# Optimization experiments

Hardware: AMD Instinct MI355X
Metric: run time of the kernel (lower is better)

## Reference

```python
import jax, jax.numpy as jnp
import numpy as np

TOP_K = 2  # k experts per token


def setup_inputs() -> dict:
    key = jax.random.key(0)
    ks = jax.random.split(key, 6)
    B, L, D, E, F = 2, 2048, 1024, 8, 4096
    x = jax.random.normal(ks[0], (B, L, D), dtype=jnp.float32)
    Wg = jax.random.normal(ks[1], (D, E), dtype=jnp.float32) * (D ** -0.5)
    W1 = jax.random.normal(ks[2], (E, D, F), dtype=jnp.float32) * (D ** -0.5)
    b1 = jnp.zeros((E, F), dtype=jnp.float32)
    W2 = jax.random.normal(ks[3], (E, F, D), dtype=jnp.float32) * (F ** -0.5)
    b2 = jnp.zeros((E, D), dtype=jnp.float32)
    return {"x": x, "Wg": Wg, "W1": W1, "b1": b1, "W2": W2, "b2": b2}


def reference(x, Wg, W1, b1, W2, b2):
    b, l, d = x.shape
    E = Wg.shape[1]
    xt = x.reshape(b * l, d)                      # (N, D)
    N = xt.shape[0]
    # Router: sigmoid gate, top-k (gate weights are NOT renormalized in the source)
    S = jax.nn.sigmoid(xt @ Wg)                   # (N, E)
    G, I = jax.lax.top_k(S, TOP_K)                # (N, k) each
    # Dense equivalent of per-expert gather-MLP-scatter: run every expert
    # on every token, then combine with the sparse top-k routing weights.
    h = jax.nn.gelu(jnp.einsum('nd,edf->enf', xt, W1) + b1[:, None, :])  # (E, N, F)
    y = jnp.einsum('enf,efd->end', h, W2) + b2[:, None, :]               # (E, N, D)
    # combine[n, e] = sum of gate values for slots routed to expert e
    combine = jnp.zeros((N, E), dtype=x.dtype).at[jnp.arange(N)[:, None], I].add(G)
    out = jnp.einsum('ne,end->nd', combine, y)    # (N, D)
    return out.reshape(b, l, d)
```

## Files before the change

### kernel.cpp

```cpp
#include <hip/hip_runtime.h>
#include <math.h>

typedef __bf16 bf16_t;
typedef __attribute__((ext_vector_type(8))) __bf16 bf16x8;
typedef __attribute__((ext_vector_type(4))) __bf16 bf16x4;
typedef __attribute__((ext_vector_type(4))) float f32x4;

#define NTOK 4096
#define DDIM 1024
#define FDIM 4096
#define NEXP 8
#define CAP  4096
#define HROWS (2*NTOK + 128)
#define NPAIR (2*NTOK)
#define MAXB 72

#define PREP_BLOCKS 2048
#define PREP_UNITS 13312

#define GLOAD_LDS16(g, l) \
  __builtin_amdgcn_global_load_lds((__attribute__((address_space(1))) void*)(g), \
                                   (__attribute__((address_space(3))) void*)(l), 16, 0, 0)

__device__ __forceinline__ float fast_gelu(float v) {
  float u = 0.7978845608028654f * (v + 0.044715f * v * v * v);
  float uc = fminf(fmaxf(u, -10.f), 10.f);
  float t = __builtin_amdgcn_exp2f(2.885390081777927f * uc);
  float th = (t - 1.f) * __builtin_amdgcn_rcpf(t + 1.f);
  return 0.5f * v * (1.0f + th);
}

__device__ __forceinline__ void reg_transpose(const float* __restrict__ ip,
                                              bf16_t* __restrict__ op,
                                              int R, int C, int r0, int c0,
                                              int t) {
  const int w = t >> 6;
  const int lane = t & 63;
  const int g = lane >> 4;
  const int m = lane & 15;
  const int rr = r0 + w * 32 + 8 * g;
  const int cc = c0 + 4 * m;
  f32x4 v[8];
#pragma unroll
  for (int ri = 0; ri < 8; ri++)
    v[ri] = *(const f32x4*)(ip + (size_t)(rr + ri) * C + cc);
#pragma unroll
  for (int ci = 0; ci < 4; ci++) {
    bf16x8 o;
#pragma unroll
    for (int ri = 0; ri < 8; ri++) o[ri] = (bf16_t)v[ri][ci];
    *(bf16x8*)(op + (size_t)(cc + ci) * R + rr) = o;
  }
}

__global__ __launch_bounds__(256) void prep_kernel(
    const float* __restrict__ W1, const float* __restrict__ W2,
    const float* __restrict__ x, const float* __restrict__ Wg,
    bf16_t* __restrict__ wt1, bf16_t* __restrict__ wt2,
    bf16_t* __restrict__ xbf, int* __restrict__ tokL, int* __restrict__ cnts,
    int* __restrict__ pairE, int* __restrict__ pairS, float* __restrict__ pairG) {
  const int t = threadIdx.x;
  for (int u = blockIdx.x; u < PREP_UNITS; u += PREP_BLOCKS) {
    if (u < 4096) {
      int e = u >> 9, ti = u & 511;
      int r0 = (ti & 7) * 128, c0 = (ti >> 3) * 64;
      reg_transpose(W1 + (size_t)e * DDIM * FDIM, wt1 + (size_t)e * DDIM * FDIM,
                    DDIM, FDIM, r0, c0, t);
    } else if (u < 8192) {
      int b0 = u - 4096;
      int e = b0 >> 9, ti = b0 & 511;
      int r0 = (ti & 31) * 128, c0 = (ti >> 5) * 64;
      reg_transpose(W2 + (size_t)e * FDIM * DDIM, wt2 + (size_t)e * FDIM * DDIM,
                    FDIM, DDIM, r0, c0, t);
    } else if (u < 12288) {
      int i = (u - 8192) * 256 + t;
      float4 v = ((const float4*)x)[i];
      bf16x4 o;
      o.x = (bf16_t)v.x; o.y = (bf16_t)v.y; o.z = (bf16_t)v.z; o.w = (bf16_t)v.w;
      ((bf16x4*)xbf)[i] = o;
    } else {
      int b0 = u - 12288;
      int wid = t >> 6, lane = t & 63;
      int n = b0 * 4 + wid;
      const float* xr = x + (size_t)n * DDIM;
      double acc[NEXP];
#pragma unroll
      for (int e = 0; e < NEXP; e++) acc[e] = 0.0;
      for (int i = 0; i < DDIM / 64; i++) {
        int d = i * 64 + lane;
        float xv = xr[d];
        const float* wr = Wg + (size_t)d * NEXP;
#pragma unroll
        for (int e = 0; e < NEXP; e++) acc[e] += (double)xv * (double)wr[e];
      }
#pragma unroll
      for (int e = 0; e < NEXP; e++) {
        double v = acc[e];
#pragma unroll
        for (int off = 32; off; off >>= 1) v += __shfl_xor(v, off);
        acc[e] = v;
      }
      if (lane == 0) {
        int i1 = -1, i2 = -1;
        double s1 = -1e300, s2 = -1e300;
#pragma unroll
        for (int e = 0; e < NEXP; e++) {
          double v = acc[e];
          if (v > s1) { s2 = s1; i2 = i1; s1 = v; i1 = e; }
          else if (v > s2) { s2 = v; i2 = e; }
        }
        float g1 = 1.0f / (1.0f + expf((float)(-s1)));
        float g2 = 1.0f / (1.0f + expf((float)(-s2)));
        int p1 = atomicAdd(&cnts[i1], 1);
        tokL[i1 * CAP + p1] = n;
        int p2 = atomicAdd(&cnts[i2], 1);
        tokL[i2 * CAP + p2] = n;
        pairE[2 * n] = i1; pairS[2 * n] = p1; pairG[2 * n] = g1;
        pairE[2 * n + 1] = i2; pairS[2 * n + 1] = p2; pairG[2 * n + 1] = g2;
      }
    }
  }
}

__global__ void offs_kernel(const int* __restrict__ cnts, int* __restrict__ offs,
                            int* __restrict__ blkE, int* __restrict__ blkS) {
  if (threadIdx.x == 0) {
    int s = 0, nb = 0;
    for (int e = 0; e < NEXP; e++) {
      offs[e] = s;
      for (int st = 0; st < cnts[e]; st += 128) { blkE[nb] = e; blkS[nb] = st; nb++; }
      s += cnts[e];
    }
    offs[NEXP] = s;
    for (; nb < MAXB; nb++) { blkE[nb] = NEXP; blkS[nb] = 0; }
  }
}

__global__ __launch_bounds__(256) void gemm1_kernel(
    const bf16_t* __restrict__ xbf, const bf16_t* __restrict__ wt1,
    const float* __restrict__ b1, const int* __restrict__ tokL,
    const int* __restrict__ cnts, const int* __restrict__ offs,
    const int* __restrict__ blkE, const int* __restrict__ blkS,
    bf16_t* __restrict__ H) {
  const int e = blkE[blockIdx.y];
  if (e >= NEXP) return;
  const int m0 = blkS[blockIdx.y];
  const int cnt = cnts[e];
  const int n0 = blockIdx.x * 128;
  const int t = threadIdx.x;

  __shared__ alignas(16) bf16_t As[128 * 32];
  __shared__ alignas(16) bf16_t Bs[128 * 32];

  const int sr = t >> 2;
  const int sc = (t & 3) * 8;
  const int r0 = m0 + sr, r1 = m0 + sr + 64;
  const int tok0 = (r0 < cnt) ? tokL[e * CAP + r0] : 0;
  const int tok1 = (r1 < cnt) ? tokL[e * CAP + r1] : 0;
  const bf16_t* gA0 = xbf + (size_t)tok0 * DDIM + sc;
  const bf16_t* gA1 = xbf + (size_t)tok1 * DDIM + sc;
  const bf16_t* wte = wt1 + (size_t)e * FDIM * DDIM;
  const bf16_t* gB0 = wte + (size_t)(n0 + sr) * DDIM + sc;
  const bf16_t* gB1 = wte + (size_t)(n0 + sr + 64) * DDIM + sc;
  bf16_t* lA0 = As + t * 8; bf16_t* lA1 = As + 2048 + t * 8;
  bf16_t* lB0 = Bs + t * 8; bf16_t* lB1 = Bs + 2048 + t * 8;

  const int lane = t & 63, w = t >> 6;
  const int wm = (w >> 1) * 64, wn = (w & 1) * 64;
  const int lid = lane & 15, quad = lane >> 4;

  f32x4 acc[4][4] = {};
  for (int kk = 0; kk < DDIM; kk += 32) {
    GLOAD_LDS16(gA0 + kk, lA0);
    GLOAD_LDS16(gA1 + kk, lA1);
    GLOAD_LDS16(gB0 + kk, lB0);
    GLOAD_LDS16(gB1 + kk, lB1);
    __syncthreads();
    bf16x8 af[4], bfm[4];
#pragma unroll
    for (int i = 0; i < 4; i++)
      af[i] = *(const bf16x8*)(As + (wm + i * 16 + lid) * 32 + quad * 8);
#pragma unroll
    for (int j = 0; j < 4; j++)
      bfm[j] = *(const bf16x8*)(Bs + (wn + j * 16 + lid) * 32 + quad * 8);
#pragma unroll
    for (int i = 0; i < 4; i++)
#pragma unroll
      for (int j = 0; j < 4; j++)
        acc[i][j] = __builtin_amdgcn_mfma_f32_16x16x32_bf16(af[i], bfm[j], acc[i][j], 0, 0, 0);
    __syncthreads();
  }

  const float* b1e = b1 + (size_t)e * FDIM;
  const int offe = offs[e];
#pragma unroll
  for (int i = 0; i < 4; i++) {
#pragma unroll
    for (int reg = 0; reg < 4; reg++) {
      int pos = m0 + wm + i * 16 + quad * 4 + reg;
      if (pos >= cnt) continue;
      size_t hrow = (size_t)(offe + pos);
#pragma unroll
      for (int j = 0; j < 4; j++) {
        int col = n0 + wn + j * 16 + lid;
        float v = acc[i][j][reg] + b1e[col];
        H[hrow * FDIM + col] = (bf16_t)fast_gelu(v);
      }
    }
  }
}

__global__ __launch_bounds__(256) void gemm2_kernel(
    const bf16_t* __restrict__ H, const bf16_t* __restrict__ wt2,
    const int* __restrict__ cnts, const int* __restrict__ offs,
    const int* __restrict__ blkE, const int* __restrict__ blkS,
    float* __restrict__ Y0, float* __restrict__ Y1) {
  const int bi = blockIdx.y >> 1;
  const int split = blockIdx.y & 1;
  const int e = blkE[bi];
  if (e >= NEXP) return;
  const int m0 = blkS[bi];
  const int cnt = cnts[e];
  const int n0 = blockIdx.x * 128;
  const int t = threadIdx.x;
  const int offe = offs[e];
  const int k0 = split * (FDIM / 2);

  __shared__ alignas(16) bf16_t As[128 * 32];
  __shared__ alignas(16) bf16_t Bs[128 * 32];

  const int sr = t >> 2;
  const int sc = (t & 3) * 8;
  const bf16_t* gA0 = H + (size_t)(offe + m0 + sr) * FDIM + sc + k0;
  const bf16_t* gA1 = H + (size_t)(offe + m0 + sr + 64) * FDIM + sc + k0;
  const bf16_t* wte = wt2 + (size_t)e * DDIM * FDIM;
  const bf16_t* gB0 = wte + (size_t)(n0 + sr) * FDIM + sc + k0;
  const bf16_t* gB1 = wte + (size_t)(n0 + sr + 64) * FDIM + sc + k0;
  bf16_t* lA0 = As + t * 8; bf16_t* lA1 = As + 2048 + t * 8;
  bf16_t* lB0 = Bs + t * 8; bf16_t* lB1 = Bs + 2048 + t * 8;

  const int lane = t & 63, w = t >> 6;
  const int wm = (w >> 1) * 64, wn = (w & 1) * 64;
  const int lid = lane & 15, quad = lane >> 4;

  f32x4 acc[4][4] = {};
  for (int kk = 0; kk < FDIM / 2; kk += 32) {
    GLOAD_LDS16(gA0 + kk, lA0);
    GLOAD_LDS16(gA1 + kk, lA1);
    GLOAD_LDS16(gB0 + kk, lB0);
    GLOAD_LDS16(gB1 + kk, lB1);
    __syncthreads();
    bf16x8 af[4], bfm[4];
#pragma unroll
    for (int i = 0; i < 4; i++)
      af[i] = *(const bf16x8*)(As + (wm + i * 16 + lid) * 32 + quad * 8);
#pragma unroll
    for (int j = 0; j < 4; j++)
      bfm[j] = *(const bf16x8*)(Bs + (wn + j * 16 + lid) * 32 + quad * 8);
#pragma unroll
    for (int i = 0; i < 4; i++)
#pragma unroll
      for (int j = 0; j < 4; j++)
        acc[i][j] = __builtin_amdgcn_mfma_f32_16x16x32_bf16(af[i], bfm[j], acc[i][j], 0, 0, 0);
    __syncthreads();
  }

  float* Ye = split ? Y1 : Y0;
#pragma unroll
  for (int i = 0; i < 4; i++) {
#pragma unroll
    for (int reg = 0; reg < 4; reg++) {
      int pos = m0 + wm + i * 16 + quad * 4 + reg;
      if (pos >= cnt) continue;
      float* yrow = Ye + (size_t)(offe + pos) * DDIM;
#pragma unroll
      for (int j = 0; j < 4; j++) {
        int col = n0 + wn + j * 16 + lid;
        yrow[col] = acc[i][j][reg];
      }
    }
  }
}

__global__ __launch_bounds__(256) void combine_kernel(
    const float* __restrict__ Y0, const float* __restrict__ Y1,
    const float* __restrict__ b2, const int* __restrict__ pairE,
    const int* __restrict__ pairS, const float* __restrict__ pairG,
    const int* __restrict__ offs, float4* __restrict__ out4) {
  const int n = blockIdx.x;
  const int e1 = pairE[2 * n], e2 = pairE[2 * n + 1];
  const int r1 = offs[e1] + pairS[2 * n];
  const int r2 = offs[e2] + pairS[2 * n + 1];
  const float g1 = pairG[2 * n], g2 = pairG[2 * n + 1];
  const int t = threadIdx.x;
  const float4* ya0 = (const float4*)(Y0 + (size_t)r1 * DDIM);
  const float4* ya1 = (const float4*)(Y1 + (size_t)r1 * DDIM);
  const float4* yb0 = (const float4*)(Y0 + (size_t)r2 * DDIM);
  const float4* yb1 = (const float4*)(Y1 + (size_t)r2 * DDIM);
  const float4* ba = (const float4*)(b2 + (size_t)e1 * DDIM);
  const float4* bb = (const float4*)(b2 + (size_t)e2 * DDIM);
  float4 a0 = ya0[t], a1 = ya1[t], c0 = yb0[t], c1 = yb1[t];
  float4 pa = ba[t], pb = bb[t];
  float4 o;
  o.x = g1 * (a0.x + a1.x + pa.x) + g2 * (c0.x + c1.x + pb.x);
  o.y = g1 * (a0.y + a1.y + pa.y) + g2 * (c0.y + c1.y + pb.y);
  o.z = g1 * (a0.z + a1.z + pa.z) + g2 * (c0.z + c1.z + pb.z);
  o.w = g1 * (a0.w + a1.w + pa.w) + g2 * (c0.w + c1.w + pb.w);
  out4[(size_t)n * (DDIM / 4) + t] = o;
}

extern "C" void kernel_launch(void* const* d_in, const int* in_sizes, int n_in,
                              void* d_out, int out_size, void* d_ws, size_t ws_size,
                              hipStream_t stream) {
  const float* x  = (const float*)d_in[0];
  const float* Wg = (const float*)d_in[1];
  const float* W1 = (const float*)d_in[2];
  const float* b1 = (const float*)d_in[3];
  const float* W2 = (const float*)d_in[4];
  const float* b2 = (const float*)d_in[5];
  float* out = (float*)d_out;

  char* ws = (char*)d_ws;
  size_t off = 0;
  auto alloc = [&](size_t bytes) -> void* {
    void* p = (void*)(ws + off);
    off += (bytes + 255) & ~(size_t)255;
    return p;
  };
  bf16_t* xbf   = (bf16_t*)alloc((size_t)NTOK * DDIM * 2);
  bf16_t* wt1   = (bf16_t*)alloc((size_t)NEXP * FDIM * DDIM * 2);
  bf16_t* wt2   = (bf16_t*)alloc((size_t)NEXP * DDIM * FDIM * 2);
  bf16_t* H     = (bf16_t*)alloc((size_t)HROWS * FDIM * 2);
  int*    tokL  = (int*)alloc((size_t)NEXP * CAP * 4);
  int*    pairE = (int*)alloc((size_t)NPAIR * 4);
  int*    pairS = (int*)alloc((size_t)NPAIR * 4);
  float*  pairG = (float*)alloc((size_t)NPAIR * 4);
  int*    cnts  = (int*)alloc(64);
  int*    offs  = (int*)alloc(64);
  int*    blkE  = (int*)alloc(MAXB * 4);
  int*    blkS  = (int*)alloc(MAXB * 4);
  if (off > ws_size) return;

  float* Y0 = (float*)wt1;
  float* Y1 = Y0 + (size_t)8192 * DDIM;

  hipMemsetAsync(cnts, 0, 64, stream);
  prep_kernel<<<PREP_BLOCKS, 256, 0, stream>>>(W1, W2, x, Wg, wt1, wt2, xbf, tokL,
                                               cnts, pairE, pairS, pairG);
  offs_kernel<<<1, 64, 0, stream>>>(cnts, offs, blkE, blkS);
  gemm1_kernel<<<dim3(FDIM / 128, MAXB), 256, 0, stream>>>(
      xbf, wt1, b1, tokL, cnts, offs, blkE, blkS, H);
  gemm2_kernel<<<dim3(DDIM / 128, MAXB * 2), 256, 0, stream>>>(
      H, wt2, cnts, offs, blkE, blkS, Y0, Y1);
  combine_kernel<<<NTOK, 256, 0, stream>>>(Y0, Y1, b2, pairE, pairS, pairG, offs,
                                           (float4*)out);
}
```

Baseline: 670.5 us.

## Swizzle GEMM block order for L2 locality and drop gemm2 split-K

Remaps block indices in both GEMM kernels so that consecutive blocks dispatched to the same XCD share weight or activation tiles in L2. Removes the two-way split-K in the second GEMM, so each block covers the full F dimension and writes a single Y buffer. The combine kernel then reads one partial instead of two per routed slot. This cuts Y write and read traffic, but halves the gemm2 grid and doubles its per-block serial K loop, which may hurt occupancy and tail balance.

Result: slower. 685.8 us (+2.3%).

```diff
diff --git a/kernel.cpp b/kernel.cpp
--- a/kernel.cpp
+++ b/kernel.cpp
@@ -142,11 +142,15 @@
     const int* __restrict__ cnts, const int* __restrict__ offs,
     const int* __restrict__ blkE, const int* __restrict__ blkS,
     bf16_t* __restrict__ H) {
-  const int e = blkE[blockIdx.y];
+  const int bid = blockIdx.x + 32 * blockIdx.y;
+  const int swz = (bid & 7) * 288 + (bid >> 3);
+  const int by = swz % 72;
+  const int bx = swz / 72;
+  const int e = blkE[by];
   if (e >= NEXP) return;
-  const int m0 = blkS[blockIdx.y];
+  const int m0 = blkS[by];
   const int cnt = cnts[e];
-  const int n0 = blockIdx.x * 128;
+  const int n0 = bx * 128;
   const int t = threadIdx.x;
 
   __shared__ alignas(16) bf16_t As[128 * 32];
@@ -214,28 +218,29 @@
     const bf16_t* __restrict__ H, const bf16_t* __restrict__ wt2,
     const int* __restrict__ cnts, const int* __restrict__ offs,
     const int* __restrict__ blkE, const int* __restrict__ blkS,
-    float* __restrict__ Y0, float* __restrict__ Y1) {
-  const int bi = blockIdx.y >> 1;
-  const int split = blockIdx.y & 1;
-  const int e = blkE[bi];
+    float* __restrict__ Y) {
+  const int bid = blockIdx.x + 8 * blockIdx.y;
+  const int swz = (bid & 7) * 72 + (bid >> 3);
+  const int bx = swz & 7;
+  const int by = swz >> 3;
+  const int e = blkE[by];
   if (e >= NEXP) return;
-  const int m0 = blkS[bi];
+  const int m0 = blkS[by];
   const int cnt = cnts[e];
-  const int n0 = blockIdx.x * 128;
+  const int n0 = bx * 128;
   const int t = threadIdx.x;
   const int offe = offs[e];
-  const int k0 = split * (FDIM / 2);
 
   __shared__ alignas(16) bf16_t As[128 * 32];
   __shared__ alignas(16) bf16_t Bs[128 * 32];
 
   const int sr = t >> 2;
   const int sc = (t & 3) * 8;
-  const bf16_t* gA0 = H + (size_t)(offe + m0 + sr) * FDIM + sc + k0;
-  const bf16_t* gA1 = H + (size_t)(offe + m0 + sr + 64) * FDIM + sc + k0;
+  const bf16_t* gA0 = H + (size_t)(offe + m0 + sr) * FDIM + sc;
+  const bf16_t* gA1 = H + (size_t)(offe + m0 + sr + 64) * FDIM + sc;
   const bf16_t* wte = wt2 + (size_t)e * DDIM * FDIM;
-  const bf16_t* gB0 = wte + (size_t)(n0 + sr) * FDIM + sc + k0;
-  const bf16_t* gB1 = wte + (size_t)(n0 + sr + 64) * FDIM + sc + k0;
+  const bf16_t* gB0 = wte + (size_t)(n0 + sr) * FDIM + sc;
+  const bf16_t* gB1 = wte + (size_t)(n0 + sr + 64) * FDIM + sc;
   bf16_t* lA0 = As + t * 8; bf16_t* lA1 = As + 2048 + t * 8;
   bf16_t* lB0 = Bs + t * 8; bf16_t* lB1 = Bs + 2048 + t * 8;
 
@@ -244,7 +249,7 @@
   const int lid = lane & 15, quad = lane >> 4;
 
   f32x4 acc[4][4] = {};
-  for (int kk = 0; kk < FDIM / 2; kk += 32) {
+  for (int kk = 0; kk < FDIM; kk += 32) {
     GLOAD_LDS16(gA0 + kk, lA0);
     GLOAD_LDS16(gA1 + kk, lA1);
     GLOAD_LDS16(gB0 + kk, lB0);
@@ -265,14 +270,13 @@
     __syncthreads();
   }
 
-  float* Ye = split ? Y1 : Y0;
 #pragma unroll
   for (int i = 0; i < 4; i++) {
 #pragma unroll
     for (int reg = 0; reg < 4; reg++) {
       int pos = m0 + wm + i * 16 + quad * 4 + reg;
       if (pos >= cnt) continue;
-      float* yrow = Ye + (size_t)(offe + pos) * DDIM;
+      float* yrow = Y + (size_t)(offe + pos) * DDIM;
 #pragma unroll
       for (int j = 0; j < 4; j++) {
         int col = n0 + wn + j * 16 + lid;
@@ -283,29 +287,27 @@
 }
 
 __global__ __launch_bounds__(256) void combine_kernel(
-    const float* __restrict__ Y0, const float* __restrict__ Y1,
-    const float* __restrict__ b2, const int* __restrict__ pairE,
-    const int* __restrict__ pairS, const float* __restrict__ pairG,
-    const int* __restrict__ offs, float4* __restrict__ out4) {
+    const float* __restrict__ Y, const float* __restrict__ b2,
+    const int* __restrict__ pairE, const int* __restrict__ pairS,
+    const float* __restrict__ pairG, const int* __restrict__ offs,
+    float4* __restrict__ out4) {
   const int n = blockIdx.x;
   const int e1 = pairE[2 * n], e2 = pairE[2 * n + 1];
   const int r1 = offs[e1] + pairS[2 * n];
   const int r2 = offs[e2] + pairS[2 * n + 1];
   const float g1 = pairG[2 * n], g2 = pairG[2 * n + 1];
   const int t = threadIdx.x;
-  const float4* ya0 = (const float4*)(Y0 + (size_t)r1 * DDIM);
-  const float4* ya1 = (const float4*)(Y1 + (size_t)r1 * DDIM);
-  const float4* yb0 = (const float4*)(Y0 + (size_t)r2 * DDIM);
-  const float4* yb1 = (const float4*)(Y1 + (size_t)r2 * DDIM);
+  const float4* ya = (const float4*)(Y + (size_t)r1 * DDIM);
+  const float4* yb = (const float4*)(Y + (size_t)r2 * DDIM);
   const float4* ba = (const float4*)(b2 + (size_t)e1 * DDIM);
   const float4* bb = (const float4*)(b2 + (size_t)e2 * DDIM);
-  float4 a0 = ya0[t], a1 = ya1[t], c0 = yb0[t], c1 = yb1[t];
+  float4 a0 = ya[t], c0 = yb[t];
   float4 pa = ba[t], pb = bb[t];
   float4 o;
-  o.x = g1 * (a0.x + a1.x + pa.x) + g2 * (c0.x + c1.x + pb.x);
-  o.y = g1 * (a0.y + a1.y + pa.y) + g2 * (c0.y + c1.y + pb.y);
-  o.z = g1 * (a0.z + a1.z + pa.z) + g2 * (c0.z + c1.z + pb.z);
-  o.w = g1 * (a0.w + a1.w + pa.w) + g2 * (c0.w + c1.w + pb.w);
+  o.x = g1 * (a0.x + pa.x) + g2 * (c0.x + pb.x);
+  o.y = g1 * (a0.y + pa.y) + g2 * (c0.y + pb.y);
+  o.z = g1 * (a0.z + pa.z) + g2 * (c0.z + pb.z);
+  o.w = g1 * (a0.w + pa.w) + g2 * (c0.w + pb.w);
   out4[(size_t)n * (DDIM / 4) + t] = o;
 }
 
@@ -341,8 +343,7 @@
   int*    blkS  = (int*)alloc(MAXB * 4);
   if (off > ws_size) return;
 
-  float* Y0 = (float*)wt1;
-  float* Y1 = Y0 + (size_t)8192 * DDIM;
+  float* Y = (float*)wt1;
 
   hipMemsetAsync(cnts, 0, 64, stream);
   prep_kernel<<<PREP_BLOCKS, 256, 0, stream>>>(W1, W2, x, Wg, wt1, wt2, xbf, tokL,
@@ -350,8 +351,8 @@
   offs_kernel<<<1, 64, 0, stream>>>(cnts, offs, blkE, blkS);
   gemm1_kernel<<<dim3(FDIM / 128, MAXB), 256, 0, stream>>>(
       xbf, wt1, b1, tokL, cnts, offs, blkE, blkS, H);
-  gemm2_kernel<<<dim3(DDIM / 128, MAXB * 2), 256, 0, stream>>>(
-      H, wt2, cnts, offs, blkE, blkS, Y0, Y1);
-  combine_kernel<<<NTOK, 256, 0, stream>>>(Y0, Y1, b2, pairE, pairS, pairG, offs,
+  gemm2_kernel<<<dim3(DDIM / 128, MAXB), 256, 0, stream>>>(
+      H, wt2, cnts, offs, blkE, blkS, Y);
+  combine_kernel<<<NTOK, 256, 0, stream>>>(Y, b2, pairE, pairS, pairG, offs,
                                            (float4*)out);
 }
```

## Double-buffer LDS tiles and swizzle block order in both MoE GEMMs

Applied to the files above, without the earlier changes.

Both expert GEMM kernels now use two LDS buffers, so the async global-to-LDS load of the next K tile is issued before the MFMA work on the current tile, leaving one barrier per iteration. Block indices are also remapped with an XCD-aware swizzle (bid&7 striding) so that blocks sharing an expert's weights or token rows land on the same XCD for L2 reuse. Cost: LDS per block doubles, which may lower occupancy. The hardcoded 288/144/72 constants tie the swizzle to a fixed grid size.

New measurement: 629.8 us. -6.1%, faster.

```diff
diff --git a/kernel.cpp b/kernel.cpp
--- a/kernel.cpp
+++ b/kernel.cpp
@@ -142,15 +142,19 @@
     const int* __restrict__ cnts, const int* __restrict__ offs,
     const int* __restrict__ blkE, const int* __restrict__ blkS,
     bf16_t* __restrict__ H) {
-  const int e = blkE[blockIdx.y];
+  const int bid = blockIdx.x + 32 * blockIdx.y;
+  const int swz = (bid & 7) * 288 + (bid >> 3);
+  const int by = swz % 72;
+  const int bx = swz / 72;
+  const int e = blkE[by];
   if (e >= NEXP) return;
-  const int m0 = blkS[blockIdx.y];
+  const int m0 = blkS[by];
   const int cnt = cnts[e];
-  const int n0 = blockIdx.x * 128;
+  const int n0 = bx * 128;
   const int t = threadIdx.x;
 
-  __shared__ alignas(16) bf16_t As[128 * 32];
-  __shared__ alignas(16) bf16_t Bs[128 * 32];
+  __shared__ alignas(16) bf16_t As[2][128 * 32];
+  __shared__ alignas(16) bf16_t Bs[2][128 * 32];
 
   const int sr = t >> 2;
   const int sc = (t & 3) * 8;
@@ -162,34 +166,42 @@
   const bf16_t* wte = wt1 + (size_t)e * FDIM * DDIM;
   const bf16_t* gB0 = wte + (size_t)(n0 + sr) * DDIM + sc;
   const bf16_t* gB1 = wte + (size_t)(n0 + sr + 64) * DDIM + sc;
-  bf16_t* lA0 = As + t * 8; bf16_t* lA1 = As + 2048 + t * 8;
-  bf16_t* lB0 = Bs + t * 8; bf16_t* lB1 = Bs + 2048 + t * 8;
 
   const int lane = t & 63, w = t >> 6;
   const int wm = (w >> 1) * 64, wn = (w & 1) * 64;
   const int lid = lane & 15, quad = lane >> 4;
 
+#define STAGE_G1(buf, kk) do { \
+    GLOAD_LDS16(gA0 + (kk), &As[buf][t * 8]); \
+    GLOAD_LDS16(gA1 + (kk), &As[buf][2048 + t * 8]); \
+    GLOAD_LDS16(gB0 + (kk), &Bs[buf][t * 8]); \
+    GLOAD_LDS16(gB1 + (kk), &Bs[buf][2048 + t * 8]); \
+  } while (0)
+
   f32x4 acc[4][4] = {};
+  STAGE_G1(0, 0);
+  __syncthreads();
+  int cur = 0;
   for (int kk = 0; kk < DDIM; kk += 32) {
-    GLOAD_LDS16(gA0 + kk, lA0);
-    GLOAD_LDS16(gA1 + kk, lA1);
-    GLOAD_LDS16(gB0 + kk, lB0);
-    GLOAD_LDS16(gB1 + kk, lB1);
-    __syncthreads();
+    if (kk + 32 < DDIM) STAGE_G1(cur ^ 1, kk + 32);
+    const bf16_t* Ac = As[cur];
+    const bf16_t* Bc = Bs[cur];
     bf16x8 af[4], bfm[4];
 #pragma unroll
     for (int i = 0; i < 4; i++)
-      af[i] = *(const bf16x8*)(As + (wm + i * 16 + lid) * 32 + quad * 8);
+      af[i] = *(const bf16x8*)(Ac + (wm + i * 16 + lid) * 32 + quad * 8);
 #pragma unroll
     for (int j = 0; j < 4; j++)
-      bfm[j] = *(const bf16x8*)(Bs + (wn + j * 16 + lid) * 32 + quad * 8);
+      bfm[j] = *(const bf16x8*)(Bc + (wn + j * 16 + lid) * 32 + quad * 8);
 #pragma unroll
     for (int i = 0; i < 4; i++)
 #pragma unroll
       for (int j = 0; j < 4; j++)
         acc[i][j] = __builtin_amdgcn_mfma_f32_16x16x32_bf16(af[i], bfm[j], acc[i][j], 0, 0, 0);
     __syncthreads();
-  }
+    cur ^= 1;
+  }
+#undef STAGE_G1
 
   const float* b1e = b1 + (size_t)e * FDIM;
   const int offe = offs[e];
@@ -215,19 +227,22 @@
     const int* __restrict__ cnts, const int* __restrict__ offs,
     const int* __restrict__ blkE, const int* __restrict__ blkS,
     float* __restrict__ Y0, float* __restrict__ Y1) {
-  const int bi = blockIdx.y >> 1;
-  const int split = blockIdx.y & 1;
-  const int e = blkE[bi];
+  const int bid = blockIdx.x + 8 * blockIdx.y;
+  const int swz = (bid & 7) * 144 + (bid >> 3);
+  const int bx = swz & 7;
+  const int split = (swz >> 3) & 1;
+  const int by = swz >> 4;
+  const int e = blkE[by];
   if (e >= NEXP) return;
-  const int m0 = blkS[bi];
+  const int m0 = blkS[by];
   const int cnt = cnts[e];
-  const int n0 = blockIdx.x * 128;
+  const int n0 = bx * 128;
   const int t = threadIdx.x;
   const int offe = offs[e];
   const int k0 = split * (FDIM / 2);
 
-  __shared__ alignas(16) bf16_t As[128 * 32];
-  __shared__ alignas(16) bf16_t Bs[128 * 32];
+  __shared__ alignas(16) bf16_t As[2][128 * 32];
+  __shared__ alignas(16) bf16_t Bs[2][128 * 32];
 
   const int sr = t >> 2;
   const int sc = (t & 3) * 8;
@@ -236,34 +251,42 @@
   const bf16_t* wte = wt2 + (size_t)e * DDIM * FDIM;
   const bf16_t* gB0 = wte + (size_t)(n0 + sr) * FDIM + sc + k0;
   const bf16_t* gB1 = wte + (size_t)(n0 + sr + 64) * FDIM + sc + k0;
-  bf16_t* lA0 = As + t * 8; bf16_t* lA1 = As + 2048 + t * 8;
-  bf16_t* lB0 = Bs + t * 8; bf16_t* lB1 = Bs + 2048 + t * 8;
 
   const int lane = t & 63, w = t >> 6;
   const int wm = (w >> 1) * 64, wn = (w & 1) * 64;
   const int lid = lane & 15, quad = lane >> 4;
 
+#define STAGE_G2(buf, kk) do { \
+    GLOAD_LDS16(gA0 + (kk), &As[buf][t * 8]); \
+    GLOAD_LDS16(gA1 + (kk), &As[buf][2048 + t * 8]); \
+    GLOAD_LDS16(gB0 + (kk), &Bs[buf][t * 8]); \
+    GLOAD_LDS16(gB1 + (kk), &Bs[buf][2048 + t * 8]); \
+  } while (0)
+
   f32x4 acc[4][4] = {};
+  STAGE_G2(0, 0);
+  __syncthreads();
+  int cur = 0;
   for (int kk = 0; kk < FDIM / 2; kk += 32) {
-    GLOAD_LDS16(gA0 + kk, lA0);
-    GLOAD_LDS16(gA1 + kk, lA1);
-    GLOAD_LDS16(gB0 + kk, lB0);
-    GLOAD_LDS16(gB1 + kk, lB1);
-    __syncthreads();
+    if (kk + 32 < FDIM / 2) STAGE_G2(cur ^ 1, kk + 32);
+    const bf16_t* Ac = As[cur];
+    const bf16_t* Bc = Bs[cur];
     bf16x8 af[4], bfm[4];
 #pragma unroll
     for (int i = 0; i < 4; i++)
-      af[i] = *(const bf16x8*)(As + (wm + i * 16 + lid) * 32 + quad * 8);
+      af[i] = *(const bf16x8*)(Ac + (wm + i * 16 + lid) * 32 + quad * 8);
 #pragma unroll
     for (int j = 0; j < 4; j++)
-      bfm[j] = *(const bf16x8*)(Bs + (wn + j * 16 + lid) * 32 + quad * 8);
+      bfm[j] = *(const bf16x8*)(Bc + (wn + j * 16 + lid) * 32 + quad * 8);
 #pragma unroll
     for (int i = 0; i < 4; i++)
 #pragma unroll
       for (int j = 0; j < 4; j++)
         acc[i][j] = __builtin_amdgcn_mfma_f32_16x16x32_bf16(af[i], bfm[j], acc[i][j], 0, 0, 0);
     __syncthreads();
-  }
+    cur ^= 1;
+  }
+#undef STAGE_G2
 
   float* Ye = split ? Y1 : Y0;
 #pragma unroll
```
